# Kernel tuning notes

Hardware: AMD Instinct MI355X
Metric: run time of the kernel (lower is better)

The kernel has to match this reference:

```python
import jax, jax.numpy as jnp
import numpy as np

H = 16      # num_heads
D = 64      # nhid (per-head dim)
SL, BS = 1024, 64
DM = 1024   # keys_dim == query_dim == values_dim

def setup_inputs() -> dict:
    key = jax.random.key(0)
    k1, k2, k3, k4, k5 = jax.random.split(key, 5)
    return {
        "query":  jax.random.normal(k1, (BS, DM), dtype=jnp.float32),
        "keys":   jax.random.normal(k2, (SL, BS, DM), dtype=jnp.float32),
        "values": jax.random.normal(k3, (SL, BS, DM), dtype=jnp.float32),
        "Wq":     jax.random.normal(k4, (H * D, DM), dtype=jnp.float32) * 0.02,
        "Wk":     jax.random.normal(k5, (H * D, DM), dtype=jnp.float32) * 0.02,
    }

def reference(query, keys, values, Wq, Wk):
    bs = query.shape[0]
    sl = keys.shape[0]
    scale = jnp.asarray(np.sqrt(D), dtype=query.dtype)
    # projections (note: original module applies keys_linear to values -- a bug we replicate)
    qp = (query @ Wq.T).reshape(bs, H, D)                 # [bs, H, D]
    kp = (keys @ Wk.T).reshape(sl, bs, H, D)              # [sl, bs, H, D]
    vp = (values @ Wk.T).reshape(sl, bs, H, D)            # [sl, bs, H, D]
    # per-head scaled dot-product scores, softmax over the sequence axis (dim 0)
    scores = jnp.einsum('bhd,sbhd->sbh', qp, kp) / scale  # [sl, bs, H]
    attn = jax.nn.softmax(scores, axis=0)
    out = jnp.einsum('sbh,sbhd->bhd', attn, vp)           # [bs, H, D]
    return out.reshape(bs, H * D)
```

## Files before the change

kernel.cpp:

```cpp
#include <hip/hip_runtime.h>
#include <cstddef>
#include <cstdint>

#define NH 16
#define HD 64
#define SLEN 1024
#define NB 64
#define DMODEL 1024

#define DOT4_ACC(acc, k, q) \
  acc = fmaf((k).x, (q).x, fmaf((k).y, (q).y, fmaf((k).z, (q).z, fmaf((k).w, (q).w, (acc)))))

#define FMA4_BCAST(accv, qv, w0_, w1_, w2_, w3_) do { \
  (accv).x = fmaf((qv).x, (w0_).x, fmaf((qv).y, (w1_).x, fmaf((qv).z, (w2_).x, fmaf((qv).w, (w3_).x, (accv).x)))); \
  (accv).y = fmaf((qv).x, (w0_).y, fmaf((qv).y, (w1_).y, fmaf((qv).z, (w2_).y, fmaf((qv).w, (w3_).y, (accv).y)))); \
  (accv).z = fmaf((qv).x, (w0_).z, fmaf((qv).y, (w1_).z, fmaf((qv).z, (w2_).z, fmaf((qv).w, (w3_).z, (accv).z)))); \
  (accv).w = fmaf((qv).x, (w0_).w, fmaf((qv).y, (w1_).w, fmaf((qv).z, (w2_).w, fmaf((qv).w, (w3_).w, (accv).w)))); \
} while (0)

__device__ __forceinline__ float wred_sum(float v) {
#pragma unroll
  for (int off = 32; off; off >>= 1) v += __shfl_xor(v, off, 64);
  return v;
}

__device__ __forceinline__ void gload16(const float* g, float* lds_base) {
  __builtin_amdgcn_global_load_lds(
      (const __attribute__((address_space(1))) void*)g,
      (__attribute__((address_space(3))) void*)lds_base, 16, 0, 0);
}

__global__ __launch_bounds__(256) void k0_qp(const float* __restrict__ query,
                                             const float* __restrict__ Wq,
                                             float* __restrict__ qp) {
  const int tid = threadIdx.x;
  const int w = tid >> 6, l = tid & 63;
  const int j = blockIdx.x * 4 + w;
  const float4* wr = reinterpret_cast<const float4*>(Wq + (size_t)j * DMODEL) + l * 4;
  const float4 w0 = wr[0], w1 = wr[1], w2 = wr[2], w3 = wr[3];
  for (int b = 0; b < NB; ++b) {
    const float4* qr = reinterpret_cast<const float4*>(query + (size_t)b * DMODEL) + l * 4;
    float4 q0 = qr[0], q1 = qr[1], q2 = qr[2], q3 = qr[3];
    float s = 0.f;
    DOT4_ACC(s, w0, q0); DOT4_ACC(s, w1, q1); DOT4_ACC(s, w2, q2); DOT4_ACC(s, w3, q3);
    s = wred_sum(s);
    if (l == 0) qp[(size_t)b * DMODEL + j] = s;
  }
}

__global__ __launch_bounds__(256) void k1_qt(const float* __restrict__ qp,
                                             const float* __restrict__ Wk,
                                             float* __restrict__ qt) {
  __shared__ __align__(16) float qpl[8][HD];
  const int h = blockIdx.x & 15;
  const int b0 = (blockIdx.x >> 4) * 8;
  const int tid = threadIdx.x;
  for (int f = tid; f < 8 * HD; f += 256) {
    int bi = f >> 6, d = f & 63;
    qpl[bi][d] = qp[(size_t)(b0 + bi) * DMODEL + h * HD + d];
  }
  __syncthreads();
  const int m4 = tid * 4;
  float4 acc[8];
#pragma unroll
  for (int i = 0; i < 8; ++i) acc[i] = make_float4(0.f, 0.f, 0.f, 0.f);
  const float* wbase = Wk + (size_t)(h * HD) * DMODEL + m4;
  for (int d = 0; d < HD; d += 4) {
    float4 wk0 = *reinterpret_cast<const float4*>(wbase + (size_t)(d + 0) * DMODEL);
    float4 wk1 = *reinterpret_cast<const float4*>(wbase + (size_t)(d + 1) * DMODEL);
    float4 wk2 = *reinterpret_cast<const float4*>(wbase + (size_t)(d + 2) * DMODEL);
    float4 wk3 = *reinterpret_cast<const float4*>(wbase + (size_t)(d + 3) * DMODEL);
#pragma unroll
    for (int bi = 0; bi < 8; ++bi) {
      float4 q = *reinterpret_cast<const float4*>(&qpl[bi][d]);
      FMA4_BCAST(acc[bi], q, wk0, wk1, wk2, wk3);
    }
  }
#pragma unroll
  for (int bi = 0; bi < 8; ++bi)
    *reinterpret_cast<float4*>(qt + ((size_t)(b0 + bi) * NH + h) * DMODEL + m4) = acc[bi];
}

__global__ __launch_bounds__(256) void k2_scores(const float* __restrict__ keys,
                                                 const float* __restrict__ qt,
                                                 float* __restrict__ scp) {
  __shared__ __align__(16) float kb[2][64 * 64];
  __shared__ __align__(16) float qb[2][NH * 64];
  const int b  = blockIdx.x & 63;
  const int st = (blockIdx.x >> 6) & 15;
  const int mh = blockIdx.x >> 10;
  const int tid = threadIdx.x, w = tid >> 6, l = tid & 63;
  const int hg = l & 3;
  const int sg = l >> 2;
  const int s0 = st * 64;
  const size_t rowstride = (size_t)NB * DMODEL;
  const float* kbase = keys + ((size_t)s0 * NB + b) * DMODEL + mh * 512;
  const float* qbase = qt + (size_t)b * NH * DMODEL + mh * 512;
  const int srow_lo = l >> 4;
  const int sslot   = l & 15;
  const int qh = w * 4 + (l >> 4);

#define K2_STAGE(buf_, ch_) do {                                               \
    _Pragma("unroll")                                                          \
    for (int i_ = 0; i_ < 4; ++i_) {                                           \
      const int row_ = i_ * 16 + w * 4 + srow_lo;                              \
      gload16(kbase + (size_t)row_ * rowstride + (ch_) * 64 +                  \
                  ((sslot ^ (row_ & 7)) << 2),                                 \
              &kb[buf_][(i_ * 16 + w * 4) * 64]);                              \
    }                                                                          \
    gload16(qbase + (size_t)qh * DMODEL + (ch_) * 64 + (sslot << 2),           \
            &qb[buf_][w * 4 * 64]);                                            \
  } while (0)

  float acc[4][4];
#pragma unroll
  for (int si = 0; si < 4; ++si)
#pragma unroll
    for (int hh = 0; hh < 4; ++hh) acc[si][hh] = 0.f;

  K2_STAGE(0, 0);
  __syncthreads();
  for (int ch = 0; ch < 8; ++ch) {
    const int buf = ch & 1;
    if (ch + 1 < 8) K2_STAGE(buf ^ 1, ch + 1);
    float4 kv[4][4];
#pragma unroll
    for (int si = 0; si < 4; ++si) {
      const int row = si * 16 + sg;
      const int sw = (row & 7) << 2;
#pragma unroll
      for (int j = 0; j < 4; ++j)
        kv[si][j] = *reinterpret_cast<const float4*>(
            &kb[buf][row * 64 + ((hg * 4 + 16 * j) ^ sw)]);
    }
#pragma unroll
    for (int hh = 0; hh < 4; ++hh) {
      const float* qrow = &qb[buf][(w * 4 + hh) * 64 + hg * 4];
      float4 q0 = *reinterpret_cast<const float4*>(qrow);
      float4 q1 = *reinterpret_cast<const float4*>(qrow + 16);
      float4 q2 = *reinterpret_cast<const float4*>(qrow + 32);
      float4 q3 = *reinterpret_cast<const float4*>(qrow + 48);
#pragma unroll
      for (int si = 0; si < 4; ++si) {
        DOT4_ACC(acc[si][hh], kv[si][0], q0);
        DOT4_ACC(acc[si][hh], kv[si][1], q1);
        DOT4_ACC(acc[si][hh], kv[si][2], q2);
        DOT4_ACC(acc[si][hh], kv[si][3], q3);
      }
    }
    __syncthreads();
  }
#undef K2_STAGE
#pragma unroll
  for (int si = 0; si < 4; ++si)
#pragma unroll
    for (int hh = 0; hh < 4; ++hh) {
      acc[si][hh] += __shfl_xor(acc[si][hh], 1, 64);
      acc[si][hh] += __shfl_xor(acc[si][hh], 2, 64);
    }
  const float scale = 0.125f;
  float* plane = scp + (size_t)mh * NB * NH * SLEN;
#pragma unroll
  for (int si = 0; si < 4; ++si) {
    float r = hg == 0 ? acc[si][0] : hg == 1 ? acc[si][1]
            : hg == 2 ? acc[si][2] : acc[si][3];
    plane[((size_t)b * NH + w * 4 + hg) * SLEN + s0 + si * 16 + sg] = r * scale;
  }
}

__global__ __launch_bounds__(256) void k_sm(float* __restrict__ sc0,
                                            const float* __restrict__ sc1) {
  __shared__ float red[8];
  const int tid = threadIdx.x, w = tid >> 6, l = tid & 63;
  float* p0 = sc0 + (size_t)blockIdx.x * SLEN;
  const float* p1 = sc1 + (size_t)blockIdx.x * SLEN;
  float4 xa = reinterpret_cast<const float4*>(p0)[tid];
  float4 xb = reinterpret_cast<const float4*>(p1)[tid];
  float4 x = make_float4(xa.x + xb.x, xa.y + xb.y, xa.z + xb.z, xa.w + xb.w);
  float mx = fmaxf(fmaxf(x.x, x.y), fmaxf(x.z, x.w));
#pragma unroll
  for (int off = 32; off; off >>= 1) mx = fmaxf(mx, __shfl_xor(mx, off, 64));
  if (l == 0) red[w] = mx;
  __syncthreads();
  mx = fmaxf(fmaxf(red[0], red[1]), fmaxf(red[2], red[3]));
  float4 e;
  e.x = __expf(x.x - mx); e.y = __expf(x.y - mx);
  e.z = __expf(x.z - mx); e.w = __expf(x.w - mx);
  float sum = e.x + e.y + e.z + e.w;
  sum = wred_sum(sum);
  if (l == 0) red[4 + w] = sum;
  __syncthreads();
  sum = red[4] + red[5] + red[6] + red[7];
  const float inv = 1.f / sum;
  e.x *= inv; e.y *= inv; e.z *= inv; e.w *= inv;
  reinterpret_cast<float4*>(p0)[tid] = e;
}

template <int NCH>
__global__ __launch_bounds__(256) void k3_cpart(const float* __restrict__ values,
                                                const float* __restrict__ attn,
                                                float* __restrict__ cp) {
  constexpr int SC = SLEN / NCH;
  __shared__ __align__(16) float vb[2][4][DMODEL];
  __shared__ __align__(16) float al[NH][SC];
  const int b = blockIdx.x & 63;
  const int ch = blockIdx.x >> 6;
  const int s0 = ch * SC;
  const int tid = threadIdx.x, w = tid >> 6, l = tid & 63;
  for (int f = tid; f < NH * (SC / 4); f += 256) {
    int hh = f / (SC / 4), c4 = (f % (SC / 4)) * 4;
    *reinterpret_cast<float4*>(&al[hh][c4]) = *reinterpret_cast<const float4*>(
        attn + ((size_t)b * NH + hh) * SLEN + s0 + c4);
  }
  const int m4 = tid * 4;
  float4 acc[NH];
#pragma unroll
  for (int i = 0; i < NH; ++i) acc[i] = make_float4(0.f, 0.f, 0.f, 0.f);
  const size_t rowstride = (size_t)NB * DMODEL;
  const float* vbase = values + ((size_t)s0 * NB + b) * DMODEL;

#define K3_STAGE(buf_, g_) do {                                               \
    const float* rg_ = vbase + (size_t)((g_) * 4 + w) * rowstride;            \
    _Pragma("unroll")                                                         \
    for (int j_ = 0; j_ < 4; ++j_)                                            \
      gload16(rg_ + j_ * 256 + l * 4, &vb[buf_][w][j_ * 256]);                \
  } while (0)

  K3_STAGE(0, 0);
  __syncthreads();
  for (int g = 0; g < SC / 4; ++g) {
    const int buf = g & 1;
    if (g + 1 < SC / 4) K3_STAGE(buf ^ 1, g + 1);
    float4 v0 = *reinterpret_cast<const float4*>(&vb[buf][0][m4]);
    float4 v1 = *reinterpret_cast<const float4*>(&vb[buf][1][m4]);
    float4 v2 = *reinterpret_cast<const float4*>(&vb[buf][2][m4]);
    float4 v3 = *reinterpret_cast<const float4*>(&vb[buf][3][m4]);
#pragma unroll
    for (int hh = 0; hh < NH; ++hh) {
      float4 av = *reinterpret_cast<const float4*>(&al[hh][g * 4]);
      FMA4_BCAST(acc[hh], av, v0, v1, v2, v3);
    }
    __syncthreads();
  }
#undef K3_STAGE
#pragma unroll
  for (int hh = 0; hh < NH; ++hh)
    *reinterpret_cast<float4*>(cp + (((size_t)ch * NB + b) * NH + hh) * DMODEL + m4) = acc[hh];
}

template <int NCH>
__global__ __launch_bounds__(256) void k4_out(const float* __restrict__ cp,
                                              const float* __restrict__ Wk,
                                              float* __restrict__ out) {
  __shared__ __align__(16) float cl[4 * DMODEL];
  const int h = blockIdx.x & 15;
  const int b0 = (blockIdx.x >> 4) * 4;
  const int tid = threadIdx.x, w = tid >> 6, l = tid & 63;
  for (int f = tid; f < 4 * DMODEL / 4; f += 256) {
    int bi = f >> 8, m4 = (f & 255) * 4;
    float4 s = make_float4(0.f, 0.f, 0.f, 0.f);
#pragma unroll
    for (int ch = 0; ch < NCH; ++ch) {
      float4 t = *reinterpret_cast<const float4*>(
          cp + (((size_t)ch * NB + b0 + bi) * NH + h) * DMODEL + m4);
      s.x += t.x; s.y += t.y; s.z += t.z; s.w += t.w;
    }
    *reinterpret_cast<float4*>(&cl[bi * DMODEL + m4]) = s;
  }
  __syncthreads();
  float4 c[4][4];
#pragma unroll
  for (int bi = 0; bi < 4; ++bi)
#pragma unroll
    for (int k = 0; k < 4; ++k)
      c[bi][k] = *reinterpret_cast<const float4*>(&cl[bi * DMODEL + l * 16 + k * 4]);
  for (int jj = 0; jj < 16; ++jj) {
    const int d = w * 16 + jj;
    const float4* wr = reinterpret_cast<const float4*>(Wk + (size_t)(h * HD + d) * DMODEL) + l * 4;
    const float4 w0 = wr[0], w1 = wr[1], w2 = wr[2], w3 = wr[3];
#pragma unroll
    for (int bi = 0; bi < 4; ++bi) {
      float s = 0.f;
      DOT4_ACC(s, w0, c[bi][0]); DOT4_ACC(s, w1, c[bi][1]);
      DOT4_ACC(s, w2, c[bi][2]); DOT4_ACC(s, w3, c[bi][3]);
      s = wred_sum(s);
      if (l == 0) out[(size_t)(b0 + bi) * (NH * HD) + h * HD + d] = s;
    }
  }
}

extern "C" void kernel_launch(void* const* d_in, const int* in_sizes, int n_in,
                              void* d_out, int out_size, void* d_ws, size_t ws_size,
                              hipStream_t stream) {
  const float* query  = (const float*)d_in[0];
  const float* keys   = (const float*)d_in[1];
  const float* values = (const float*)d_in[2];
  const float* Wq     = (const float*)d_in[3];
  const float* Wk     = (const float*)d_in[4];
  float* out = (float*)d_out;

  float* W   = (float*)d_ws;
  float* qp  = W;
  float* qt  = qp + (size_t)NB * DMODEL;
  float* sc0 = qt + (size_t)NB * NH * DMODEL;
  float* sc1 = sc0 + (size_t)NB * NH * SLEN;
  float* cp  = sc1 + (size_t)NB * NH * SLEN;

  const size_t base_floats = (size_t)NB * DMODEL + (size_t)NB * NH * DMODEL
                           + 2 * (size_t)NB * NH * SLEN;

  k0_qp<<<256, 256, 0, stream>>>(query, Wq, qp);
  k1_qt<<<128, 256, 0, stream>>>(qp, Wk, qt);
  k2_scores<<<2048, 256, 0, stream>>>(keys, qt, sc0);
  k_sm<<<NB * NH, 256, 0, stream>>>(sc0, sc1);

  const size_t chunk_floats = (size_t)NB * NH * DMODEL;
  if (ws_size >= (base_floats + 16 * chunk_floats) * sizeof(float)) {
    k3_cpart<16><<<16 * NB, 256, 0, stream>>>(values, sc0, cp);
    k4_out<16><<<NH * (NB / 4), 256, 0, stream>>>(cp, Wk, out);
  } else if (ws_size >= (base_floats + 8 * chunk_floats) * sizeof(float)) {
    k3_cpart<8><<<8 * NB, 256, 0, stream>>>(values, sc0, cp);
    k4_out<8><<<NH * (NB / 4), 256, 0, stream>>>(cp, Wk, out);
  } else {
    k3_cpart<4><<<4 * NB, 256, 0, stream>>>(values, sc0, cp);
    k4_out<4><<<NH * (NB / 4), 256, 0, stream>>>(cp, Wk, out);
  }
}
```

Before: 244.5 us.

## Split Q projection kernels across more blocks and remap score thread layout

```diff
diff --git a/kernel.cpp b/kernel.cpp
--- a/kernel.cpp
+++ b/kernel.cpp
@@ -35,10 +35,12 @@
                                              float* __restrict__ qp) {
   const int tid = threadIdx.x;
   const int w = tid >> 6, l = tid & 63;
-  const int j = blockIdx.x * 4 + w;
+  const int jq = blockIdx.x & 255;
+  const int bq = blockIdx.x >> 8;
+  const int j = jq * 4 + w;
   const float4* wr = reinterpret_cast<const float4*>(Wq + (size_t)j * DMODEL) + l * 4;
   const float4 w0 = wr[0], w1 = wr[1], w2 = wr[2], w3 = wr[3];
-  for (int b = 0; b < NB; ++b) {
+  for (int b = bq * 16; b < bq * 16 + 16; ++b) {
     const float4* qr = reinterpret_cast<const float4*>(query + (size_t)b * DMODEL) + l * 4;
     float4 q0 = qr[0], q1 = qr[1], q2 = qr[2], q3 = qr[3];
     float s = 0.f;
@@ -51,34 +53,29 @@
 __global__ __launch_bounds__(256) void k1_qt(const float* __restrict__ qp,
                                              const float* __restrict__ Wk,
                                              float* __restrict__ qt) {
-  __shared__ __align__(16) float qpl[8][HD];
+  __shared__ __align__(16) float qpl[2][HD];
   const int h = blockIdx.x & 15;
-  const int b0 = (blockIdx.x >> 4) * 8;
+  const int b0 = (blockIdx.x >> 4) * 2;
   const int tid = threadIdx.x;
-  for (int f = tid; f < 8 * HD; f += 256) {
-    int bi = f >> 6, d = f & 63;
-    qpl[bi][d] = qp[(size_t)(b0 + bi) * DMODEL + h * HD + d];
-  }
+  if (tid < 2 * HD) qpl[tid >> 6][tid & 63] =
+      qp[(size_t)(b0 + (tid >> 6)) * DMODEL + h * HD + (tid & 63)];
   __syncthreads();
   const int m4 = tid * 4;
-  float4 acc[8];
-#pragma unroll
-  for (int i = 0; i < 8; ++i) acc[i] = make_float4(0.f, 0.f, 0.f, 0.f);
+  float4 acc0 = make_float4(0.f, 0.f, 0.f, 0.f);
+  float4 acc1 = make_float4(0.f, 0.f, 0.f, 0.f);
   const float* wbase = Wk + (size_t)(h * HD) * DMODEL + m4;
   for (int d = 0; d < HD; d += 4) {
     float4 wk0 = *reinterpret_cast<const float4*>(wbase + (size_t)(d + 0) * DMODEL);
     float4 wk1 = *reinterpret_cast<const float4*>(wbase + (size_t)(d + 1) * DMODEL);
     float4 wk2 = *reinterpret_cast<const float4*>(wbase + (size_t)(d + 2) * DMODEL);
     float4 wk3 = *reinterpret_cast<const float4*>(wbase + (size_t)(d + 3) * DMODEL);
-#pragma unroll
-    for (int bi = 0; bi < 8; ++bi) {
-      float4 q = *reinterpret_cast<const float4*>(&qpl[bi][d]);
-      FMA4_BCAST(acc[bi], q, wk0, wk1, wk2, wk3);
-    }
-  }
-#pragma unroll
-  for (int bi = 0; bi < 8; ++bi)
-    *reinterpret_cast<float4*>(qt + ((size_t)(b0 + bi) * NH + h) * DMODEL + m4) = acc[bi];
+    float4 qa = *reinterpret_cast<const float4*>(&qpl[0][d]);
+    float4 qb = *reinterpret_cast<const float4*>(&qpl[1][d]);
+    FMA4_BCAST(acc0, qa, wk0, wk1, wk2, wk3);
+    FMA4_BCAST(acc1, qb, wk0, wk1, wk2, wk3);
+  }
+  *reinterpret_cast<float4*>(qt + ((size_t)(b0 + 0) * NH + h) * DMODEL + m4) = acc0;
+  *reinterpret_cast<float4*>(qt + ((size_t)(b0 + 1) * NH + h) * DMODEL + m4) = acc1;
 }
 
 __global__ __launch_bounds__(256) void k2_scores(const float* __restrict__ keys,
@@ -92,79 +89,72 @@
   const int tid = threadIdx.x, w = tid >> 6, l = tid & 63;
   const int hg = l & 3;
   const int sg = l >> 2;
+  const int row = w * 16 + sg;
   const int s0 = st * 64;
   const size_t rowstride = (size_t)NB * DMODEL;
   const float* kbase = keys + ((size_t)s0 * NB + b) * DMODEL + mh * 512;
   const float* qbase = qt + (size_t)b * NH * DMODEL + mh * 512;
-  const int srow_lo = l >> 4;
-  const int sslot   = l & 15;
-  const int qh = w * 4 + (l >> 4);
+  const int srow4 = l >> 4;
+  const int sslot = l & 15;
 
 #define K2_STAGE(buf_, ch_) do {                                               \
     _Pragma("unroll")                                                          \
     for (int i_ = 0; i_ < 4; ++i_) {                                           \
-      const int row_ = i_ * 16 + w * 4 + srow_lo;                              \
-      gload16(kbase + (size_t)row_ * rowstride + (ch_) * 64 +                  \
-                  ((sslot ^ (row_ & 7)) << 2),                                 \
-              &kb[buf_][(i_ * 16 + w * 4) * 64]);                              \
+      const int r_ = w * 16 + i_ * 4 + srow4;                                  \
+      gload16(kbase + (size_t)r_ * rowstride + (ch_) * 64 +                    \
+                  ((sslot ^ (r_ & 7)) << 2),                                   \
+              &kb[buf_][(w * 16 + i_ * 4) * 64]);                              \
     }                                                                          \
-    gload16(qbase + (size_t)qh * DMODEL + (ch_) * 64 + (sslot << 2),           \
+      \
+    gload16(qbase + (size_t)(w * 4 + srow4) * DMODEL + (ch_) * 64 +            \
+                (sslot << 2),                                                  \
             &qb[buf_][w * 4 * 64]);                                            \
   } while (0)
 
-  float acc[4][4];
-#pragma unroll
-  for (int si = 0; si < 4; ++si)
-#pragma unroll
-    for (int hh = 0; hh < 4; ++hh) acc[si][hh] = 0.f;
+  float acc[NH];
+#pragma unroll
+  for (int hh = 0; hh < NH; ++hh) acc[hh] = 0.f;
 
   K2_STAGE(0, 0);
   __syncthreads();
   for (int ch = 0; ch < 8; ++ch) {
     const int buf = ch & 1;
     if (ch + 1 < 8) K2_STAGE(buf ^ 1, ch + 1);
-    float4 kv[4][4];
-#pragma unroll
-    for (int si = 0; si < 4; ++si) {
-      const int row = si * 16 + sg;
-      const int sw = (row & 7) << 2;
-#pragma unroll
-      for (int j = 0; j < 4; ++j)
-        kv[si][j] = *reinterpret_cast<const float4*>(
-            &kb[buf][row * 64 + ((hg * 4 + 16 * j) ^ sw)]);
-    }
-#pragma unroll
-    for (int hh = 0; hh < 4; ++hh) {
-      const float* qrow = &qb[buf][(w * 4 + hh) * 64 + hg * 4];
+    float4 kv0 = *reinterpret_cast<const float4*>(
+        &kb[buf][row * 64 + (((hg + 0) ^ (row & 7)) << 2)]);
+    float4 kv1 = *reinterpret_cast<const float4*>(
+        &kb[buf][row * 64 + (((hg + 4) ^ (row & 7)) << 2)]);
+    float4 kv2 = *reinterpret_cast<const float4*>(
+        &kb[buf][row * 64 + (((hg + 8) ^ (row & 7)) << 2)]);
+    float4 kv3 = *reinterpret_cast<const float4*>(
+        &kb[buf][row * 64 + (((hg + 12) ^ (row & 7)) << 2)]);
+#pragma unroll
+    for (int hh = 0; hh < NH; ++hh) {
+      const float* qrow = &qb[buf][hh * 64 + hg * 4];
       float4 q0 = *reinterpret_cast<const float4*>(qrow);
       float4 q1 = *reinterpret_cast<const float4*>(qrow + 16);
       float4 q2 = *reinterpret_cast<const float4*>(qrow + 32);
       float4 q3 = *reinterpret_cast<const float4*>(qrow + 48);
-#pragma unroll
-      for (int si = 0; si < 4; ++si) {
-        DOT4_ACC(acc[si][hh], kv[si][0], q0);
-        DOT4_ACC(acc[si][hh], kv[si][1], q1);
-        DOT4_ACC(acc[si][hh], kv[si][2], q2);
-        DOT4_ACC(acc[si][hh], kv[si][3], q3);
-      }
+      DOT4_ACC(acc[hh], kv0, q0);
+      DOT4_ACC(acc[hh], kv1, q1);
+      DOT4_ACC(acc[hh], kv2, q2);
+      DOT4_ACC(acc[hh], kv3, q3);
     }
     __syncthreads();
   }
 #undef K2_STAGE
 #pragma unroll
-  for (int si = 0; si < 4; ++si)
-#pragma unroll
-    for (int hh = 0; hh < 4; ++hh) {
-      acc[si][hh] += __shfl_xor(acc[si][hh], 1, 64);
-      acc[si][hh] += __shfl_xor(acc[si][hh], 2, 64);
-    }
+  for (int hh = 0; hh < NH; ++hh) {
+    acc[hh] += __shfl_xor(acc[hh], 1, 64);
+    acc[hh] += __shfl_xor(acc[hh], 2, 64);
+  }
   const float scale = 0.125f;
   float* plane = scp + (size_t)mh * NB * NH * SLEN;
 #pragma unroll
-  for (int si = 0; si < 4; ++si) {
-    float r = hg == 0 ? acc[si][0] : hg == 1 ? acc[si][1]
-            : hg == 2 ? acc[si][2] : acc[si][3];
-    plane[((size_t)b * NH + w * 4 + hg) * SLEN + s0 + si * 16 + sg] = r * scale;
+  for (int jh = 0; jh < 4; ++jh) {
+    float r = hg == 0 ? acc[jh] : hg == 1 ? acc[4 + jh]
+            : hg == 2 ? acc[8 + jh] : acc[12 + jh];
+    plane[((size_t)b * NH + hg * 4 + jh) * SLEN + s0 + row] = r * scale;
   }
 }
 
@@ -309,8 +299,8 @@
   const size_t base_floats = (size_t)NB * DMODEL + (size_t)NB * NH * DMODEL
                            + 2 * (size_t)NB * NH * SLEN;
 
-  k0_qp<<<256, 256, 0, stream>>>(query, Wq, qp);
-  k1_qt<<<128, 256, 0, stream>>>(qp, Wk, qt);
+  k0_qp<<<1024, 256, 0, stream>>>(query, Wq, qp);
+  k1_qt<<<512, 256, 0, stream>>>(qp, Wk, qt);
   k2_scores<<<2048, 256, 0, stream>>>(keys, qt, sc0);
   k_sm<<<NB * NH, 256, 0, stream>>>(sc0, sc1);
 
```

After: 220.8 us. 1.11x faster.
